# Kernel optimization log

Measured on AMD Instinct MI355X. Metric: run time of the kernel, lower is better.

## Reference

```python
import jax, jax.numpy as jnp
import numpy as np

N = 128   # n_features == out_dim (required by the Christoffel permutes)
H = 256   # MLP hidden width of forward_func
B = 16    # batch size (state_batch is [2B, N])
EPS_G = 1e-4
EPS_DG = 1e-6
EPS_V = 1e-6


def setup_inputs() -> dict:
    key = jax.random.key(0)
    ks = jax.random.split(key, 6)
    return {
        "t": jax.random.uniform(ks[0], (), dtype=jnp.float32),
        "state_batch": jax.random.normal(ks[1], (2 * B, N), dtype=jnp.float32) * 0.1,
        "x0_batch": jax.random.normal(ks[2], (B, N), dtype=jnp.float32),
        "x1_batch": jax.random.normal(ks[3], (B, N), dtype=jnp.float32),
        "W1": jax.random.normal(ks[4], (N, H), dtype=jnp.float32) / np.float32(np.sqrt(N)),
        "b1": jnp.zeros((H,), dtype=jnp.float32),
        "W2": jax.random.normal(ks[5], (H, N), dtype=jnp.float32) / np.float32(np.sqrt(H)),
        "b2": jnp.zeros((N,), dtype=jnp.float32),
    }


def reference(t, state_batch, x0_batch, x1_batch, W1, b1, W2, b2):
    def f(x):  # forward_func, per-sample: [N] -> [N]
        return jnp.tanh(x @ W1 + b1) @ W2 + b2

    def metric(x):  # G(x) = J J^T + 1e-4 I, per-sample: [N] -> [N, N]
        J = jax.jacrev(f)(x)                      # [N, N], matches per-output grad loop
        return J @ J.T + EPS_G * jnp.eye(N, dtype=x.dtype)

    deviation, dev_velocity = jnp.split(state_batch, 2, axis=0)  # each [B, N]
    window = 4.0 * t * (1.0 - t)
    # x along the perturbed straight path
    x = x0_batch + t * (x1_batch - x0_batch) + window * deviation  # [B, N]

    # dG[b, i, j, k] = dG_ij/dx_k -- replaces the out_dim^2 autograd.grad loop
    dG = jax.vmap(jax.jacfwd(metric))(x)  # [B, N, N, N]
    nrm = jnp.sqrt(jnp.sum(dG * dG, axis=(1, 2, 3), keepdims=True))
    dG = dG / (nrm + EPS_DG)

    # Christoffel-like symbols
    Gamma = 0.5 * (dG + jnp.transpose(dG, (0, 2, 1, 3)) - jnp.transpose(dG, (0, 3, 1, 2)))
    a = -jnp.einsum('bijk,bj,bk->bi', Gamma, dev_velocity, dev_velocity)
    a = a / (jnp.linalg.norm(dev_velocity, axis=1, keepdims=True) + EPS_V)

    restoration = -0.1 * deviation
    return jnp.concatenate([dev_velocity, a + restoration], axis=0)  # [2B, N]
```

## Files before the change

### kernel.cpp

```cpp
#include <hip/hip_runtime.h>
#include <math.h>


static constexpr int OFF_W2T  = 0;
static constexpr int OFF_S    = 32768;
static constexpr int OFF_Q    = 98304;
static constexpr int OFF_D    = 163840;
static constexpr int OFF_C    = 167936;
static constexpr int OFF_UV   = 172032;
static constexpr int OFF_AV   = 176128;
static constexpr int OFF_VN   = 180224;
static constexpr int OFF_PART = 180240;
static constexpr int OFF_PT   = 180992;
static constexpr int OFF_PN   = 705536;

__global__ __launch_bounds__(256) void k_stage1(const float* __restrict__ tptr,
                                                const float* __restrict__ state,
                                                const float* __restrict__ x0,
                                                const float* __restrict__ x1,
                                                const float* __restrict__ W1,
                                                const float* __restrict__ b1,
                                                const float* __restrict__ W2,
                                                float* __restrict__ ws,
                                                float* __restrict__ out) {
    __shared__ __align__(16) float smem[2 * 32 * 34];
    int blk = blockIdx.x;
    int tid = threadIdx.x;

    if (blk < 64) {
        float* Ai = smem;
        float* Aj = smem + 1088;
        int m0 = (blk >> 3) * 32, n0 = (blk & 7) * 32;
        int lx = tid & 31, lr = tid >> 5;
        int tx = tid & 15, ty = tid >> 4;
        float a00 = 0, a01 = 0, a10 = 0, a11 = 0;
        for (int kc = 0; kc < 128; kc += 32) {
            #pragma unroll
            for (int i = 0; i < 4; ++i) {
                int k = lr + 8 * i;
                Ai[k * 34 + lx] = W1[(kc + k) * 256 + m0 + lx];
                Aj[k * 34 + lx] = W1[(kc + k) * 256 + n0 + lx];
            }
            __syncthreads();
            #pragma unroll
            for (int k = 0; k < 32; ++k) {
                float2 a = *(const float2*)&Ai[k * 34 + 2 * ty];
                float2 b = *(const float2*)&Aj[k * 34 + 2 * tx];
                a00 += a.x * b.x; a01 += a.x * b.y;
                a10 += a.y * b.x; a11 += a.y * b.y;
            }
            __syncthreads();
        }
        float* S = ws + OFF_S;
        int m = m0 + 2 * ty, n = n0 + 2 * tx;
        S[m * 256 + n]           = a00;
        S[m * 256 + n + 1]       = a01;
        S[(m + 1) * 256 + n]     = a10;
        S[(m + 1) * 256 + n + 1] = a11;
    } else if (blk < 128) {
        float* Xi = smem;
        float* Xj = smem + 1088;
        int bq = blk - 64;
        int m0 = (bq >> 3) * 32, n0 = (bq & 7) * 32;
        int lx = tid & 31, lr = tid >> 5;
        int tx = tid & 15, ty = tid >> 4;
        float a00 = 0, a01 = 0, a10 = 0, a11 = 0;
        for (int kc = 0; kc < 128; kc += 32) {
            #pragma unroll
            for (int i = 0; i < 4; ++i) {
                Xi[lx * 34 + lr + 8 * i] = W2[(m0 + lr + 8 * i) * 128 + kc + lx];
                Xj[lx * 34 + lr + 8 * i] = W2[(n0 + lr + 8 * i) * 128 + kc + lx];
            }
            __syncthreads();
            #pragma unroll
            for (int k = 0; k < 32; ++k) {
                float2 a = *(const float2*)&Xi[k * 34 + 2 * ty];
                float2 b = *(const float2*)&Xj[k * 34 + 2 * tx];
                a00 += a.x * b.x; a01 += a.x * b.y;
                a10 += a.y * b.x; a11 += a.y * b.y;
            }
            __syncthreads();
        }
        float* Q = ws + OFF_Q;
        int m = m0 + 2 * ty, n = n0 + 2 * tx;
        Q[m * 256 + n]           = a00;
        Q[m * 256 + n + 1]       = a01;
        Q[(m + 1) * 256 + n]     = a10;
        Q[(m + 1) * 256 + n + 1] = a11;
    } else if (blk < 160) {
        float* tile = smem;
        int b2 = blk - 128;
        int c0 = (b2 & 3) * 32, r0 = (b2 >> 2) * 32;
        int tx = tid & 31, ty = tid >> 5;
        #pragma unroll
        for (int i = 0; i < 32; i += 8)
            tile[(ty + i) * 33 + tx] = W2[(r0 + ty + i) * 128 + c0 + tx];
        __syncthreads();
        float* W2T = ws + OFF_W2T;
        #pragma unroll
        for (int i = 0; i < 32; i += 8)
            W2T[(c0 + ty + i) * 256 + r0 + tx] = tile[tx * 33 + ty + i];
    } else {
        int b = blk - 160;
        float* xs  = smem;
        float* vs  = smem + 128;
        float* red = smem + 256;
        float t = tptr[0];
        float w = 4.f * t * (1.f - t);
        if (tid < 128) {
            float dev = state[b * 128 + tid];
            float v   = state[(16 + b) * 128 + tid];
            float xv  = x0[b * 128 + tid] + t * (x1[b * 128 + tid] - x0[b * 128 + tid]) + w * dev;
            xs[tid] = xv;
            vs[tid] = v;
            out[b * 128 + tid] = v;
            red[tid] = v * v;
        }
        __syncthreads();
        for (int s = 64; s > 0; s >>= 1) {
            if (tid < s) red[tid] += red[tid + s];
            __syncthreads();
        }
        if (tid == 0) ws[OFF_VN + b] = sqrtf(red[0]);

        int m = tid;
        float h = b1[m], uvm = 0.f;
        #pragma unroll 8
        for (int k = 0; k < 128; ++k) {
            float wv = W1[k * 256 + m];
            h   += xs[k] * wv;
            uvm += vs[k] * wv;
        }
        float z  = tanhf(h);
        float dd = 1.f - z * z;
        float cc = -2.f * z * dd;
        const float4* w2r = (const float4*)&W2[m * 128];
        const float4* vs4 = (const float4*)vs;
        float avm = 0.f;
        #pragma unroll 8
        for (int j4 = 0; j4 < 32; ++j4) {
            float4 ww = w2r[j4];
            float4 vv = vs4[j4];
            avm += ww.x * vv.x + ww.y * vv.y + ww.z * vv.z + ww.w * vv.w;
        }
        ws[OFF_D  + b * 256 + m] = dd;
        ws[OFF_C  + b * 256 + m] = cc;
        ws[OFF_UV + b * 256 + m] = uvm;
        ws[OFF_AV + b * 256 + m] = avm;
    }
}

__global__ __launch_bounds__(64) void k_pmat2(const float* __restrict__ Smat,
                                              const float* __restrict__ dall,
                                              const float* __restrict__ W2,
                                              float* __restrict__ PT,
                                              float* __restrict__ Pn) {
    __shared__ __align__(16) float ST[32 * 36];
    __shared__ __align__(16) float YT[32 * 36];
    int b = blockIdx.z, mt = blockIdx.y, jt = blockIdx.x;
    int m0 = mt * 32, j0 = jt * 32;
    const float* dvec = dall + b * 256;
    int tid = threadIdx.x;
    int nr = tid >> 3, l4 = (tid & 7) * 4;
    int ty = tid >> 3, tx = tid & 7;
    float acc[4][4] = {};
    for (int nc = 0; nc < 256; nc += 32) {
        #pragma unroll
        for (int i = 0; i < 4; ++i) {
            int n = nr + 8 * i;
            *(float4*)&ST[n * 36 + l4] = *(const float4*)&Smat[(nc + n) * 256 + m0 + l4];
            float dn = dvec[nc + n];
            float4 wv = *(const float4*)&W2[(nc + n) * 128 + j0 + l4];
            wv.x *= dn; wv.y *= dn; wv.z *= dn; wv.w *= dn;
            *(float4*)&YT[n * 36 + l4] = wv;
        }
        __syncthreads();
        #pragma unroll
        for (int n = 0; n < 32; ++n) {
            float4 a  = *(const float4*)&ST[n * 36 + 4 * ty];
            float4 bb = *(const float4*)&YT[n * 36 + 4 * tx];
            float av[4] = {a.x, a.y, a.z, a.w};
            float bv[4] = {bb.x, bb.y, bb.z, bb.w};
            #pragma unroll
            for (int ii = 0; ii < 4; ++ii)
                #pragma unroll
                for (int jj = 0; jj < 4; ++jj)
                    acc[ii][jj] += av[ii] * bv[jj];
        }
        __syncthreads();
    }
    float* ptb = PT + b * 32768;
    float* pnb = Pn + b * 32768;
    #pragma unroll
    for (int jj = 0; jj < 4; ++jj) {
        float4 v = make_float4(acc[0][jj], acc[1][jj], acc[2][jj], acc[3][jj]);
        *(float4*)&ptb[(j0 + 4 * tx + jj) * 256 + m0 + 4 * ty] = v;
    }
    #pragma unroll
    for (int ii = 0; ii < 4; ++ii) {
        float4 v = make_float4(acc[ii][0], acc[ii][1], acc[ii][2], acc[ii][3]);
        *(float4*)&pnb[(m0 + 4 * ty + ii) * 128 + j0 + 4 * tx] = v;
    }
}

__global__ __launch_bounds__(64) void k_fnorm2(const float* __restrict__ PT,
                                               const float* __restrict__ W2T,
                                               const float* __restrict__ Smat,
                                               const float* __restrict__ Qmat,
                                               const float* __restrict__ call,
                                               float* __restrict__ partial) {
    __shared__ __align__(16) float lds[16384];
    float* PiT = lds;
    float* PjT = lds + 4096;
    float* WiT = lds + 8192;
    float* WjT = lds + 12288;
    int b = blockIdx.y;
    int idx = blockIdx.x;
    int tj = 0;
    while ((tj + 1) * (tj + 2) / 2 <= idx) ++tj;
    int ti = idx - tj * (tj + 1) / 2;
    int mi0 = ti * 32, mj0 = tj * 32;
    int tid = threadIdx.x;
    const float* ptb = PT + b * 32768;
    int jr = tid >> 3, jc4 = (tid & 7) * 4;
    #pragma unroll
    for (int it = 0; it < 16; ++it) {
        int j = jr + 8 * it;
        *(float4*)&PiT[j * 32 + jc4] = *(const float4*)&ptb[j * 256 + mi0 + jc4];
        *(float4*)&PjT[j * 32 + jc4] = *(const float4*)&ptb[j * 256 + mj0 + jc4];
        *(float4*)&WiT[j * 32 + jc4] = *(const float4*)&W2T[j * 256 + mi0 + jc4];
        *(float4*)&WjT[j * 32 + jc4] = *(const float4*)&W2T[j * 256 + mj0 + jc4];
    }
    __syncthreads();
    int ty = tid >> 3, tx = tid & 7;
    float r[4][4] = {}, f[4][4] = {}, g[4][4] = {};
    #pragma unroll 4
    for (int j = 0; j < 128; ++j) {
        float4 pi4 = *(const float4*)&PiT[j * 32 + 4 * ty];
        float4 pj4 = *(const float4*)&PjT[j * 32 + 4 * tx];
        float4 wi4 = *(const float4*)&WiT[j * 32 + 4 * ty];
        float4 wj4 = *(const float4*)&WjT[j * 32 + 4 * tx];
        float pi[4] = {pi4.x, pi4.y, pi4.z, pi4.w};
        float pj[4] = {pj4.x, pj4.y, pj4.z, pj4.w};
        float wi[4] = {wi4.x, wi4.y, wi4.z, wi4.w};
        float wj[4] = {wj4.x, wj4.y, wj4.z, wj4.w};
        #pragma unroll
        for (int ii = 0; ii < 4; ++ii)
            #pragma unroll
            for (int jj = 0; jj < 4; ++jj) {
                r[ii][jj] += pi[ii] * pj[jj];
                f[ii][jj] += pi[ii] * wj[jj];
                g[ii][jj] += pj[jj] * wi[ii];
            }
    }
    const float* cb = call + b * 256;
    float sum = 0.f;
    int mi = mi0 + 4 * ty, mj = mj0 + 4 * tx;
    float4 ce4 = *(const float4*)&cb[mj];
    float ce[4] = {ce4.x, ce4.y, ce4.z, ce4.w};
    #pragma unroll
    for (int ii = 0; ii < 4; ++ii) {
        float ci = cb[mi + ii];
        float4 S4 = *(const float4*)&Smat[(mi + ii) * 256 + mj];
        float4 Q4 = *(const float4*)&Qmat[(mi + ii) * 256 + mj];
        float Sv[4] = {S4.x, S4.y, S4.z, S4.w};
        float Qv[4] = {Q4.x, Q4.y, Q4.z, Q4.w};
        #pragma unroll
        for (int jj = 0; jj < 4; ++jj)
            sum += ci * ce[jj] * Sv[jj] * (Qv[jj] * r[ii][jj] + f[ii][jj] * g[ii][jj]);
    }
    if (ti < tj) sum *= 2.f;
    #pragma unroll
    for (int off = 32; off > 0; off >>= 1)
        sum += __shfl_down(sum, off);
    if (tid == 0) partial[b * 36 + idx] = sum;
}

__global__ __launch_bounds__(256) void k_fin2(const float* __restrict__ state,
                                              const float* __restrict__ W2,
                                              float* __restrict__ ws,
                                              float* __restrict__ out) {
    int b = blockIdx.x;
    int tid = threadIdx.x;
    __shared__ float vs[128], g1[256], g2[256], red[256];
    __shared__ float snrm;
    if (tid < 128) vs[tid] = state[(16 + b) * 128 + tid];
    red[tid] = (tid < 36) ? ws[OFF_PART + b * 36 + tid] : 0.f;
    __syncthreads();
    for (int s = 128; s > 0; s >>= 1) {
        if (tid < s) red[tid] += red[tid + s];
        __syncthreads();
    }
    if (tid == 0) snrm = sqrtf(fmaxf(2.f * red[0], 0.f));
    __syncthreads();

    const float* ptb = ws + OFF_PT + b * 32768;
    const float* pnb = ws + OFF_PN + b * 32768;
    int m = tid;
    float pv = 0.f;
    #pragma unroll 8
    for (int j = 0; j < 128; ++j)
        pv += ptb[j * 256 + m] * vs[j];
    float cc  = ws[OFF_C  + b * 256 + m];
    float uvm = ws[OFF_UV + b * 256 + m];
    float avm = ws[OFF_AV + b * 256 + m];
    g1[m] = cc * pv  * uvm;
    g2[m] = cc * avm * uvm;
    __syncthreads();

    int i = tid & 127, half = tid >> 7;
    int mmlo = half * 128;
    float raw = 0.f;
    #pragma unroll 8
    for (int mm = mmlo; mm < mmlo + 128; ++mm)
        raw += W2[mm * 128 + i] * g1[mm] + pnb[mm * 128 + i] * g2[mm];
    red[tid] = raw;
    __syncthreads();
    if (tid < 128) {
        float rawt = red[tid] + red[tid + 128];
        float vn = ws[OFF_VN + b];
        float a  = -0.5f * rawt / ((snrm + 1e-6f) * (vn + 1e-6f));
        out[(16 + b) * 128 + tid] = a - 0.1f * state[b * 128 + tid];
    }
}

extern "C" void kernel_launch(void* const* d_in, const int* in_sizes, int n_in,
                              void* d_out, int out_size, void* d_ws, size_t ws_size,
                              hipStream_t stream) {
    (void)in_sizes; (void)n_in; (void)out_size; (void)ws_size;
    const float* t     = (const float*)d_in[0];
    const float* state = (const float*)d_in[1];
    const float* x0    = (const float*)d_in[2];
    const float* x1    = (const float*)d_in[3];
    const float* W1    = (const float*)d_in[4];
    const float* b1    = (const float*)d_in[5];
    const float* W2    = (const float*)d_in[6];
    float* out = (float*)d_out;
    float* ws  = (float*)d_ws;

    k_stage1<<<176, 256, 0, stream>>>(t, state, x0, x1, W1, b1, W2, ws, out);
    k_pmat2<<<dim3(4, 8, 16), 64, 0, stream>>>(ws + OFF_S, ws + OFF_D, W2,
                                               ws + OFF_PT, ws + OFF_PN);
    k_fnorm2<<<dim3(36, 16), 64, 0, stream>>>(ws + OFF_PT, ws + OFF_W2T, ws + OFF_S,
                                              ws + OFF_Q, ws + OFF_C, ws + OFF_PART);
    k_fin2<<<16, 256, 0, stream>>>(state, W2, ws, out);
}
```

Baseline: 126.9 us.

## Fuse final stage into fnorm via last-block atomic counter, widen blocks to 256 threads

Merges the finalisation kernel into the Frobenius-norm kernel: each block atomically adds its partial sum, and the last block per batch (found with an atomic counter) computes the output. Both the P-matrix and norm kernels move from 64 to 256 threads per block. The norm kernel splits the j loop across four wavefronts and reduces the results through LDS. This removes one launch and raises occupancy, at the cost of atomics, float atomic summation order nondeterminism, and a serial tail run by one block per batch.

New measurement: 129.0 us. Within noise of the previous version (+1.7%).

```diff
diff --git a/kernel.cpp b/kernel.cpp
--- a/kernel.cpp
+++ b/kernel.cpp
@@ -10,9 +10,10 @@
 static constexpr int OFF_UV   = 172032;
 static constexpr int OFF_AV   = 176128;
 static constexpr int OFF_VN   = 180224;
-static constexpr int OFF_PART = 180240;
-static constexpr int OFF_PT   = 180992;
-static constexpr int OFF_PN   = 705536;
+static constexpr int OFF_SUM  = 180240;
+static constexpr int OFF_CNT  = 180256;
+static constexpr int OFF_PT   = 180288;
+static constexpr int OFF_PN   = 704576;
 
 __global__ __launch_bounds__(256) void k_stage1(const float* __restrict__ tptr,
                                                 const float* __restrict__ state,
@@ -107,6 +108,10 @@
         float* red = smem + 256;
         float t = tptr[0];
         float w = 4.f * t * (1.f - t);
+        if (tid == 0) {
+            ws[OFF_SUM + b] = 0.f;
+            ((int*)(ws + OFF_CNT))[b] = 0;
+        }
         if (tid < 128) {
             float dev = state[b * 128 + tid];
             float v   = state[(16 + b) * 128 + tid];
@@ -150,66 +155,68 @@
     }
 }
 
-__global__ __launch_bounds__(64) void k_pmat2(const float* __restrict__ Smat,
-                                              const float* __restrict__ dall,
-                                              const float* __restrict__ W2,
-                                              float* __restrict__ PT,
-                                              float* __restrict__ Pn) {
+__global__ __launch_bounds__(256) void k_pmat3(const float* __restrict__ Smat,
+                                               const float* __restrict__ dall,
+                                               const float* __restrict__ W2,
+                                               float* __restrict__ PT,
+                                               float* __restrict__ Pn) {
     __shared__ __align__(16) float ST[32 * 36];
-    __shared__ __align__(16) float YT[32 * 36];
+    __shared__ __align__(16) float YT[32 * 68];
     int b = blockIdx.z, mt = blockIdx.y, jt = blockIdx.x;
-    int m0 = mt * 32, j0 = jt * 32;
+    int m0 = mt * 32, j0 = jt * 64;
     const float* dvec = dall + b * 256;
     int tid = threadIdx.x;
-    int nr = tid >> 3, l4 = (tid & 7) * 4;
-    int ty = tid >> 3, tx = tid & 7;
-    float acc[4][4] = {};
+    int n = tid >> 3, c4 = (tid & 7) * 4;
+    int ty = tid >> 5, tx = tid & 31;
+    float acc[4][2] = {};
     for (int nc = 0; nc < 256; nc += 32) {
-        #pragma unroll
-        for (int i = 0; i < 4; ++i) {
-            int n = nr + 8 * i;
-            *(float4*)&ST[n * 36 + l4] = *(const float4*)&Smat[(nc + n) * 256 + m0 + l4];
-            float dn = dvec[nc + n];
-            float4 wv = *(const float4*)&W2[(nc + n) * 128 + j0 + l4];
+        *(float4*)&ST[n * 36 + c4] = *(const float4*)&Smat[(nc + n) * 256 + m0 + c4];
+        float dn = dvec[nc + n];
+        #pragma unroll
+        for (int i = 0; i < 2; ++i) {
+            int col = c4 + 32 * i;
+            float4 wv = *(const float4*)&W2[(nc + n) * 128 + j0 + col];
             wv.x *= dn; wv.y *= dn; wv.z *= dn; wv.w *= dn;
-            *(float4*)&YT[n * 36 + l4] = wv;
+            *(float4*)&YT[n * 68 + col] = wv;
         }
         __syncthreads();
-        #pragma unroll
-        for (int n = 0; n < 32; ++n) {
-            float4 a  = *(const float4*)&ST[n * 36 + 4 * ty];
-            float4 bb = *(const float4*)&YT[n * 36 + 4 * tx];
-            float av[4] = {a.x, a.y, a.z, a.w};
-            float bv[4] = {bb.x, bb.y, bb.z, bb.w};
-            #pragma unroll
-            for (int ii = 0; ii < 4; ++ii)
-                #pragma unroll
-                for (int jj = 0; jj < 4; ++jj)
-                    acc[ii][jj] += av[ii] * bv[jj];
+        #pragma unroll 8
+        for (int k = 0; k < 32; ++k) {
+            float4 a  = *(const float4*)&ST[k * 36 + 4 * ty];
+            float2 bb = *(const float2*)&YT[k * 68 + 2 * tx];
+            acc[0][0] += a.x * bb.x; acc[0][1] += a.x * bb.y;
+            acc[1][0] += a.y * bb.x; acc[1][1] += a.y * bb.y;
+            acc[2][0] += a.z * bb.x; acc[2][1] += a.z * bb.y;
+            acc[3][0] += a.w * bb.x; acc[3][1] += a.w * bb.y;
         }
         __syncthreads();
     }
     float* ptb = PT + b * 32768;
     float* pnb = Pn + b * 32768;
     #pragma unroll
-    for (int jj = 0; jj < 4; ++jj) {
+    for (int jj = 0; jj < 2; ++jj) {
         float4 v = make_float4(acc[0][jj], acc[1][jj], acc[2][jj], acc[3][jj]);
-        *(float4*)&ptb[(j0 + 4 * tx + jj) * 256 + m0 + 4 * ty] = v;
+        *(float4*)&ptb[(j0 + 2 * tx + jj) * 256 + m0 + 4 * ty] = v;
     }
     #pragma unroll
     for (int ii = 0; ii < 4; ++ii) {
-        float4 v = make_float4(acc[ii][0], acc[ii][1], acc[ii][2], acc[ii][3]);
-        *(float4*)&pnb[(m0 + 4 * ty + ii) * 128 + j0 + 4 * tx] = v;
+        float2 v = make_float2(acc[ii][0], acc[ii][1]);
+        *(float2*)&pnb[(m0 + 4 * ty + ii) * 128 + j0 + 2 * tx] = v;
     }
 }
 
-__global__ __launch_bounds__(64) void k_fnorm2(const float* __restrict__ PT,
-                                               const float* __restrict__ W2T,
-                                               const float* __restrict__ Smat,
-                                               const float* __restrict__ Qmat,
-                                               const float* __restrict__ call,
-                                               float* __restrict__ partial) {
+__global__ __launch_bounds__(256) void k_fnorm3(const float* __restrict__ PT,
+                                                const float* __restrict__ Pn,
+                                                const float* __restrict__ W2T,
+                                                const float* __restrict__ Smat,
+                                                const float* __restrict__ Qmat,
+                                                const float* __restrict__ state,
+                                                const float* __restrict__ W2,
+                                                float* __restrict__ ws,
+                                                float* __restrict__ out) {
     __shared__ __align__(16) float lds[16384];
+    __shared__ int lastflag;
+    __shared__ float snrm;
     float* PiT = lds;
     float* PjT = lds + 4096;
     float* WiT = lds + 8192;
@@ -224,18 +231,21 @@
     const float* ptb = PT + b * 32768;
     int jr = tid >> 3, jc4 = (tid & 7) * 4;
     #pragma unroll
-    for (int it = 0; it < 16; ++it) {
-        int j = jr + 8 * it;
+    for (int it = 0; it < 4; ++it) {
+        int j = jr + 32 * it;
         *(float4*)&PiT[j * 32 + jc4] = *(const float4*)&ptb[j * 256 + mi0 + jc4];
         *(float4*)&PjT[j * 32 + jc4] = *(const float4*)&ptb[j * 256 + mj0 + jc4];
         *(float4*)&WiT[j * 32 + jc4] = *(const float4*)&W2T[j * 256 + mi0 + jc4];
         *(float4*)&WjT[j * 32 + jc4] = *(const float4*)&W2T[j * 256 + mj0 + jc4];
     }
     __syncthreads();
-    int ty = tid >> 3, tx = tid & 7;
+    int w = tid >> 6, s = tid & 63;
+    int ty = s >> 3, tx = s & 7;
     float r[4][4] = {}, f[4][4] = {}, g[4][4] = {};
+    int jbase = 32 * w;
     #pragma unroll 4
-    for (int j = 0; j < 128; ++j) {
+    for (int jj = 0; jj < 32; ++jj) {
+        int j = jbase + jj;
         float4 pi4 = *(const float4*)&PiT[j * 32 + 4 * ty];
         float4 pj4 = *(const float4*)&PjT[j * 32 + 4 * tx];
         float4 wi4 = *(const float4*)&WiT[j * 32 + 4 * ty];
@@ -247,55 +257,79 @@
         #pragma unroll
         for (int ii = 0; ii < 4; ++ii)
             #pragma unroll
-            for (int jj = 0; jj < 4; ++jj) {
-                r[ii][jj] += pi[ii] * pj[jj];
-                f[ii][jj] += pi[ii] * wj[jj];
-                g[ii][jj] += pj[jj] * wi[ii];
-            }
-    }
-    const float* cb = call + b * 256;
-    float sum = 0.f;
-    int mi = mi0 + 4 * ty, mj = mj0 + 4 * tx;
-    float4 ce4 = *(const float4*)&cb[mj];
-    float ce[4] = {ce4.x, ce4.y, ce4.z, ce4.w};
-    #pragma unroll
-    for (int ii = 0; ii < 4; ++ii) {
-        float ci = cb[mi + ii];
-        float4 S4 = *(const float4*)&Smat[(mi + ii) * 256 + mj];
-        float4 Q4 = *(const float4*)&Qmat[(mi + ii) * 256 + mj];
-        float Sv[4] = {S4.x, S4.y, S4.z, S4.w};
-        float Qv[4] = {Q4.x, Q4.y, Q4.z, Q4.w};
-        #pragma unroll
-        for (int jj = 0; jj < 4; ++jj)
-            sum += ci * ce[jj] * Sv[jj] * (Qv[jj] * r[ii][jj] + f[ii][jj] * g[ii][jj]);
-    }
-    if (ti < tj) sum *= 2.f;
-    #pragma unroll
-    for (int off = 32; off > 0; off >>= 1)
-        sum += __shfl_down(sum, off);
-    if (tid == 0) partial[b * 36 + idx] = sum;
-}
-
-__global__ __launch_bounds__(256) void k_fin2(const float* __restrict__ state,
-                                              const float* __restrict__ W2,
-                                              float* __restrict__ ws,
-                                              float* __restrict__ out) {
-    int b = blockIdx.x;
-    int tid = threadIdx.x;
-    __shared__ float vs[128], g1[256], g2[256], red[256];
-    __shared__ float snrm;
+            for (int kk = 0; kk < 4; ++kk) {
+                r[ii][kk] += pi[ii] * pj[kk];
+                f[ii][kk] += pi[ii] * wj[kk];
+                g[ii][kk] += pj[kk] * wi[ii];
+            }
+    }
+    __syncthreads();
+    {
+        float* scr = lds;
+        int base = tid * 48;
+        #pragma unroll
+        for (int ii = 0; ii < 4; ++ii)
+            #pragma unroll
+            for (int kk = 0; kk < 4; ++kk) {
+                scr[base + ii * 4 + kk]      = r[ii][kk];
+                scr[base + 16 + ii * 4 + kk] = f[ii][kk];
+                scr[base + 32 + ii * 4 + kk] = g[ii][kk];
+            }
+    }
+    __syncthreads();
+    if (tid < 64) {
+        const float* scr = lds;
+        float tr[16], tf[16], tg[16];
+        #pragma unroll
+        for (int k = 0; k < 16; ++k) {
+            tr[k] = scr[tid * 48 + k]      + scr[(tid + 64) * 48 + k]
+                  + scr[(tid + 128) * 48 + k] + scr[(tid + 192) * 48 + k];
+            tf[k] = scr[tid * 48 + 16 + k]      + scr[(tid + 64) * 48 + 16 + k]
+                  + scr[(tid + 128) * 48 + 16 + k] + scr[(tid + 192) * 48 + 16 + k];
+            tg[k] = scr[tid * 48 + 32 + k]      + scr[(tid + 64) * 48 + 32 + k]
+                  + scr[(tid + 128) * 48 + 32 + k] + scr[(tid + 192) * 48 + 32 + k];
+        }
+        const float* cb = ws + OFF_C + b * 256;
+        int mi = mi0 + 4 * (tid >> 3), mj = mj0 + 4 * (tid & 7);
+        float4 ce4 = *(const float4*)&cb[mj];
+        float ce[4] = {ce4.x, ce4.y, ce4.z, ce4.w};
+        float sum = 0.f;
+        #pragma unroll
+        for (int ii = 0; ii < 4; ++ii) {
+            float ci = cb[mi + ii];
+            float4 S4 = *(const float4*)&Smat[(mi + ii) * 256 + mj];
+            float4 Q4 = *(const float4*)&Qmat[(mi + ii) * 256 + mj];
+            float Sv[4] = {S4.x, S4.y, S4.z, S4.w};
+            float Qv[4] = {Q4.x, Q4.y, Q4.z, Q4.w};
+            #pragma unroll
+            for (int kk = 0; kk < 4; ++kk)
+                sum += ci * ce[kk] * Sv[kk] * (Qv[kk] * tr[ii * 4 + kk] + tf[ii * 4 + kk] * tg[ii * 4 + kk]);
+        }
+        if (ti < tj) sum *= 2.f;
+        #pragma unroll
+        for (int off = 32; off > 0; off >>= 1)
+            sum += __shfl_down(sum, off);
+        if (tid == 0) {
+            atomicAdd(&ws[OFF_SUM + b], sum);
+            __threadfence();
+            int old = atomicAdd(((int*)(ws + OFF_CNT)) + b, 1);
+            lastflag = (old == 35) ? 1 : 0;
+        }
+    }
+    __syncthreads();
+    if (!lastflag) return;
+
+    float* vs  = lds;
+    float* g1  = lds + 128;
+    float* g2  = lds + 384;
+    float* red = lds + 640;
+    if (tid == 0) {
+        float tot = atomicAdd(&ws[OFF_SUM + b], 0.0f);
+        snrm = sqrtf(fmaxf(2.f * tot, 0.f));
+    }
     if (tid < 128) vs[tid] = state[(16 + b) * 128 + tid];
-    red[tid] = (tid < 36) ? ws[OFF_PART + b * 36 + tid] : 0.f;
-    __syncthreads();
-    for (int s = 128; s > 0; s >>= 1) {
-        if (tid < s) red[tid] += red[tid + s];
-        __syncthreads();
-    }
-    if (tid == 0) snrm = sqrtf(fmaxf(2.f * red[0], 0.f));
-    __syncthreads();
-
-    const float* ptb = ws + OFF_PT + b * 32768;
-    const float* pnb = ws + OFF_PN + b * 32768;
+    __syncthreads();
+    const float* pnb = Pn + b * 32768;
     int m = tid;
     float pv = 0.f;
     #pragma unroll 8
@@ -307,7 +341,6 @@
     g1[m] = cc * pv  * uvm;
     g2[m] = cc * avm * uvm;
     __syncthreads();
-
     int i = tid & 127, half = tid >> 7;
     int mmlo = half * 128;
     float raw = 0.f;
@@ -339,9 +372,9 @@
     float* ws  = (float*)d_ws;
 
     k_stage1<<<176, 256, 0, stream>>>(t, state, x0, x1, W1, b1, W2, ws, out);
-    k_pmat2<<<dim3(4, 8, 16), 64, 0, stream>>>(ws + OFF_S, ws + OFF_D, W2,
-                                               ws + OFF_PT, ws + OFF_PN);
-    k_fnorm2<<<dim3(36, 16), 64, 0, stream>>>(ws + OFF_PT, ws + OFF_W2T, ws + OFF_S,
-                                              ws + OFF_Q, ws + OFF_C, ws + OFF_PART);
-    k_fin2<<<16, 256, 0, stream>>>(state, W2, ws, out);
+    k_pmat3<<<dim3(2, 8, 16), 256, 0, stream>>>(ws + OFF_S, ws + OFF_D, W2,
+                                                ws + OFF_PT, ws + OFF_PN);
+    k_fnorm3<<<dim3(36, 16), 256, 0, stream>>>(ws + OFF_PT, ws + OFF_PN, ws + OFF_W2T,
+                                               ws + OFF_S, ws + OFF_Q,
+                                               state, W2, ws, out);
 }
```
